# Kernel tuning notes

Hardware: AMD Instinct MI355X
Metric: run time of the kernel (lower is better)

Reference implementation:

```python
import jax, jax.numpy as jnp
import numpy as np

EMB = 1024
HEADS = 16
WINDOW = 128


def setup_inputs() -> dict:
    key = jax.random.key(0)
    ks = jax.random.split(key, 9)
    B, N = 2, 2048
    s = 0.02
    f32 = jnp.float32
    return {
        "x": jax.random.normal(ks[0], (B, N, EMB), dtype=f32),
        "Wq": jax.random.normal(ks[1], (EMB, EMB), dtype=f32) * s,
        "bq": jnp.zeros((EMB,), dtype=f32),
        "Wk": jax.random.normal(ks[2], (EMB, EMB), dtype=f32) * s,
        "bk": jnp.zeros((EMB,), dtype=f32),
        "Wv": jax.random.normal(ks[3], (EMB, EMB), dtype=f32) * s,
        "bv": jnp.zeros((EMB,), dtype=f32),
        "Wp": jax.random.normal(ks[4], (EMB, EMB), dtype=f32) * s,
        "bp": jnp.zeros((EMB,), dtype=f32),
    }


def reference(x, Wq, bq, Wk, bk, Wv, bv, Wp, bp):
    B, N, E = x.shape
    H = HEADS
    d = E // H

    def proj(W, b):
        # torch nn.Linear: y = x @ W^T + b, then split heads -> [b, h, n, d]
        y = jnp.einsum('bne,fe->bnf', x, W) + b
        return y.reshape(B, N, H, d).transpose(0, 2, 1, 3)

    q = proj(Wq, bq)
    k = proj(Wk, bk)
    v = proj(Wv, bv)

    # full QK^T then mask out-of-window entries (faithful to original)
    energy = jnp.einsum('bhqd,bhkd->bhqk', q, k)  # [B,H,N,N]
    idx = jnp.arange(N)
    out_of_window = jnp.abs(idx[:, None] - idx[None, :]) > WINDOW  # [N,N] bool
    fmin = jnp.finfo(jnp.float32).min
    energy = jnp.where(out_of_window, fmin, energy)

    scaling = jnp.sqrt(jnp.float32(E))  # note: original scales by sqrt(emb_size)
    att = jax.nn.softmax(energy / scaling, axis=-1)

    out = jnp.einsum('bhqk,bhkd->bhqd', att, v)  # [B,H,N,d]
    out = out.transpose(0, 2, 1, 3).reshape(B, N, E)
    return jnp.einsum('bne,fe->bnf', out, Wp) + bp
```

## Files before the change

### kernel.cpp

```cpp
#include <hip/hip_runtime.h>
#include <stdint.h>

#define EMB    1024
#define NHEAD  16
#define HDIM   64
#define NSEQ   2048
#define NBATCH 2
#define WINDOW 128
#define MROWS  (NBATCH * NSEQ)

typedef __attribute__((ext_vector_type(8))) short  bf16x8;
typedef __attribute__((ext_vector_type(4))) float  f32x4;
typedef __attribute__((ext_vector_type(4))) short  short4v;

__device__ __forceinline__ unsigned short f2bf(float f) {
  union { float f; uint32_t u; } c; c.f = f;
  uint32_t u = c.u;
  u += 0x7fffu + ((u >> 16) & 1u);
  return (unsigned short)(u >> 16);
}

#define GLOAD16(g, l) __builtin_amdgcn_global_load_lds( \
    (const __attribute__((address_space(1))) void*)(g), \
    (__attribute__((address_space(3))) void*)(l), 16, 0, 0)

__global__ __launch_bounds__(256) void cvt_all(
    const float* __restrict__ x,
    const float* __restrict__ w0, const float* __restrict__ w1,
    const float* __restrict__ w2, const float* __restrict__ w3,
    unsigned short* __restrict__ xb,
    unsigned short* __restrict__ o0, unsigned short* __restrict__ o1,
    unsigned short* __restrict__ o2, unsigned short* __restrict__ o3) {
  const int i = blockIdx.x * 256 + threadIdx.x;
  const float* src; unsigned short* dst; int off;
  if (i < 1048576) { src = x; dst = xb; off = i; }
  else {
    int j = i - 1048576;
    int sel = j >> 18; off = j & 262143;
    src = sel == 0 ? w0 : sel == 1 ? w1 : sel == 2 ? w2 : w3;
    dst = sel == 0 ? o0 : sel == 1 ? o1 : sel == 2 ? o2 : o3;
  }
  float4 v = ((const float4*)src)[off];
  short4v o;
  o.x = (short)f2bf(v.x);
  o.y = (short)f2bf(v.y);
  o.z = (short)f2bf(v.z);
  o.w = (short)f2bf(v.w);
  ((short4v*)dst)[off] = o;
}

__device__ __forceinline__ void gemm_pipe(const unsigned short* __restrict__ A,
                                          const unsigned short* __restrict__ Bw,
                                          const float* __restrict__ bias,
                                          void* __restrict__ Cv,
                                          int m0, int n0, int mode, float scale) {
  constexpr int K = 1024, BK = 64, NT = K / BK;
  __shared__ char lds[2][32768];
  const int t    = threadIdx.x;
  const int lane = t & 63;
  const int wv   = t >> 6;
  const int lhi  = lane >> 4, llo = lane & 15;
  const int wr   = wv >> 1, wc = wv & 1;

  const unsigned short* gsrc[8];
  int ldsoff[8];
  #pragma unroll
  for (int li = 0; li < 8; ++li) {
    const int isB = li >= 4;
    const int c = (isB ? (li - 4) : li) * 4 + wv;
    const int P = c * 1024 + lane * 16;
    const int L = P ^ (((P >> 7) & 7) << 4);
    const int row = L >> 7, sl = (L >> 4) & 7;
    gsrc[li] = (isB ? Bw + (size_t)(n0 + row) * K : A + (size_t)(m0 + row) * K) + sl * 8;
    ldsoff[li] = isB * 16384 + c * 1024;
  }

  int aoff[2][4], boff[2][4];
  #pragma unroll
  for (int ks = 0; ks < 2; ++ks)
    #pragma unroll
    for (int f = 0; f < 4; ++f) {
      const int ar = wr * 64 + f * 16 + llo;
      aoff[ks][f] = (ar * 128 + ks * 64 + lhi * 16) ^ ((ar & 7) << 4);
      const int bc = wc * 64 + f * 16 + llo;
      boff[ks][f] = 16384 + ((bc * 128 + ks * 64 + lhi * 16) ^ ((bc & 7) << 4));
    }

  const f32x4 zero = {0.f, 0.f, 0.f, 0.f};
  f32x4 acc[4][4];
  #pragma unroll
  for (int i = 0; i < 4; ++i)
    #pragma unroll
    for (int j = 0; j < 4; ++j) acc[i][j] = zero;

  #pragma unroll
  for (int li = 0; li < 8; ++li) GLOAD16(gsrc[li], (char*)lds + ldsoff[li]);
  #pragma unroll
  for (int li = 0; li < 8; ++li) GLOAD16(gsrc[li] + BK, (char*)lds + 32768 + ldsoff[li]);

  for (int t0 = 0; t0 < NT; ++t0) {
    if (t0 + 1 < NT) asm volatile("s_waitcnt vmcnt(8)" ::: "memory");
    else             asm volatile("s_waitcnt vmcnt(0)" ::: "memory");
    asm volatile("s_barrier" ::: "memory");
    __builtin_amdgcn_sched_barrier(0);

    const char* base = (const char*)lds + (t0 & 1) * 32768;
    bf16x8 af[2][4], bg[2][4];
    #pragma unroll
    for (int ks = 0; ks < 2; ++ks)
      #pragma unroll
      for (int f = 0; f < 4; ++f) {
        af[ks][f] = *(const bf16x8*)(base + aoff[ks][f]);
        bg[ks][f] = *(const bf16x8*)(base + boff[ks][f]);
      }
    asm volatile("s_waitcnt lgkmcnt(0)" ::: "memory");
    asm volatile("s_barrier" ::: "memory");
    __builtin_amdgcn_sched_barrier(0);

    if (t0 + 2 < NT) {
      #pragma unroll
      for (int li = 0; li < 8; ++li)
        GLOAD16(gsrc[li] + (t0 + 2) * BK, (char*)lds + (t0 & 1) * 32768 + ldsoff[li]);
    }

    __builtin_amdgcn_s_setprio(1);
    #pragma unroll
    for (int ks = 0; ks < 2; ++ks)
      #pragma unroll
      for (int mf = 0; mf < 4; ++mf)
        #pragma unroll
        for (int nf = 0; nf < 4; ++nf)
          acc[mf][nf] = __builtin_amdgcn_mfma_f32_16x16x32_bf16(af[ks][mf], bg[ks][nf], acc[mf][nf], 0, 0, 0);
    __builtin_amdgcn_s_setprio(0);
  }

  const int wm = wr * 64, wn = wc * 64;
  #pragma unroll
  for (int mf = 0; mf < 4; ++mf) {
    #pragma unroll
    for (int nf = 0; nf < 4; ++nf) {
      const int col = n0 + wn + nf * 16 + llo;
      if (mode == 1) {
        const int row_base = m0 + wm + mf * 16 + lhi * 4;
        const int bb = row_base >> 11, n = row_base & 2047;
        const int hh = col >> 6, dd = col & 63;
        short4v o;
        #pragma unroll
        for (int r = 0; r < 4; ++r) o[r] = (short)f2bf((acc[mf][nf][r] + bias[col]) * scale);
        unsigned short* p = (unsigned short*)Cv +
            ((size_t)((bb * NHEAD + hh) * HDIM + dd)) * NSEQ + n;
        *(short4v*)p = o;
      } else {
        #pragma unroll
        for (int r = 0; r < 4; ++r) {
          const int row = m0 + wm + mf * 16 + lhi * 4 + r;
          const float v = (acc[mf][nf][r] + bias[col]) * scale;
          if (mode == 0) {
            const int bb = row >> 11, n = row & 2047;
            const int hh = col >> 6, dd = col & 63;
            ((unsigned short*)Cv)[((size_t)(bb * NHEAD + hh) * NSEQ + n) * HDIM + dd] = f2bf(v);
          } else {
            ((float*)Cv)[(size_t)row * EMB + col] = v;
          }
        }
      }
    }
  }
}

__global__ __launch_bounds__(256, 2) void gemm_qkv(
    const unsigned short* __restrict__ A,
    const unsigned short* __restrict__ W0, const unsigned short* __restrict__ W1,
    const unsigned short* __restrict__ W2,
    const float* __restrict__ b0, const float* __restrict__ b1, const float* __restrict__ b2,
    unsigned short* __restrict__ O0, unsigned short* __restrict__ O1,
    unsigned short* __restrict__ O2) {
  const int m0 = blockIdx.x * 128, n0 = blockIdx.y * 128;
  const unsigned short* W = (blockIdx.z == 0) ? W0 : (blockIdx.z == 1) ? W1 : W2;
  const float* bb         = (blockIdx.z == 0) ? b0 : (blockIdx.z == 1) ? b1 : b2;
  unsigned short* O       = (blockIdx.z == 0) ? O0 : (blockIdx.z == 1) ? O1 : O2;
  const int mode          = (blockIdx.z == 2) ? 1 : 0;
  const float scale       = (blockIdx.z == 0) ? 0.03125f : 1.0f;
  gemm_pipe(A, W, bb, (void*)O, m0, n0, mode, scale);
}

__global__ __launch_bounds__(256, 2) void gemm_proj(
    const unsigned short* __restrict__ A, const unsigned short* __restrict__ W,
    const float* __restrict__ bias, float* __restrict__ O) {
  gemm_pipe(A, W, bias, (void*)O, blockIdx.x * 128, blockIdx.y * 128, 2, 1.0f);
}

__global__ __launch_bounds__(256) void attn_kernel(
    const unsigned short* __restrict__ Qh, const unsigned short* __restrict__ Kh,
    const unsigned short* __restrict__ Vt, unsigned short* __restrict__ AO) {
  __shared__ unsigned short P[4][16 * 32];
  const int t = threadIdx.x;
  const int lane = t & 63, wv = t >> 6;
  const int lhi = lane >> 4, llo = lane & 15;

  const int linear = blockIdx.x + 32 * (blockIdx.y + 16 * blockIdx.z);
  const int xcd = linear & 7, pos = linear >> 3;
  const int plane = xcd * 4 + (pos >> 5);
  const int qblk = pos & 31;
  const int b = plane >> 4, h = plane & 15;
  const int q0 = qblk * 64 + wv * 16;

  const size_t pbase = (size_t)plane * NSEQ * HDIM;

  bf16x8 aq0, aq1;
  {
    const unsigned short* qp = Qh + pbase + (size_t)(q0 + llo) * HDIM + 8 * lhi;
    aq0 = *(const bf16x8*)qp;
    aq1 = *(const bf16x8*)(qp + 32);
  }

  bf16x8 vones;
  #pragma unroll
  for (int j = 0; j < 8; ++j) vones[j] = (short)0x3F80;

  const f32x4 zero = {0.f, 0.f, 0.f, 0.f};
  f32x4 accv[4];
  f32x4 s_acc = zero;
  #pragma unroll
  for (int i = 0; i < 4; ++i) accv[i] = zero;

  #pragma unroll 3
  for (int ct = 0; ct < 9; ++ct) {
    const int kb = q0 - WINDOW + ct * 32;
    f32x4 e[2];
    #pragma unroll
    for (int half = 0; half < 2; ++half) {
      int krow = kb + half * 16 + llo;
      int krc = krow < 0 ? 0 : (krow > NSEQ - 1 ? NSEQ - 1 : krow);
      const unsigned short* kp = Kh + pbase + (size_t)krc * HDIM + 8 * lhi;
      bf16x8 bk0 = *(const bf16x8*)kp;
      bf16x8 bk1 = *(const bf16x8*)(kp + 32);
      f32x4 z = zero;
      z = __builtin_amdgcn_mfma_f32_16x16x32_bf16(aq0, bk0, z, 0, 0, 0);
      z = __builtin_amdgcn_mfma_f32_16x16x32_bf16(aq1, bk1, z, 0, 0, 0);
      e[half] = z;
    }
    f32x4 p0, p1;
    #pragma unroll
    for (int half = 0; half < 2; ++half) {
      const int key = kb + half * 16 + llo;
      #pragma unroll
      for (int r = 0; r < 4; ++r) {
        const int q = q0 + lhi * 4 + r;
        const int dlt = key - q;
        const bool valid = (key >= 0) && (key < NSEQ) && (dlt <= WINDOW) && (dlt >= -WINDOW);
        const float ev = valid ? fminf(e[half][r], 40.f) : -1e30f;
        if (half == 0) p0[r] = __expf(ev); else p1[r] = __expf(ev);
      }
    }

    #pragma unroll
    for (int r = 0; r < 4; ++r) {
      P[wv][(lhi * 4 + r) * 32 + llo]      = f2bf(p0[r]);
      P[wv][(lhi * 4 + r) * 32 + 16 + llo] = f2bf(p1[r]);
    }
    const bf16x8 pa = *(const bf16x8*)&P[wv][llo * 32 + 8 * lhi];

    s_acc = __builtin_amdgcn_mfma_f32_16x16x32_bf16(pa, vones, s_acc, 0, 0, 0);

    {
      int c = kb + 8 * lhi;
      c = c < 0 ? 0 : (c > NSEQ - 8 ? NSEQ - 8 : c);
      #pragma unroll
      for (int fd = 0; fd < 4; ++fd) {
        const unsigned short* vp = Vt + pbase + (size_t)(fd * 16 + llo) * NSEQ + c;
        bf16x8 bv = *(const bf16x8*)vp;
        accv[fd] = __builtin_amdgcn_mfma_f32_16x16x32_bf16(pa, bv, accv[fd], 0, 0, 0);
      }
    }
  }

  #pragma unroll
  for (int fd = 0; fd < 4; ++fd) {
    #pragma unroll
    for (int r = 0; r < 4; ++r) {
      const float o = accv[fd][r] / s_acc[r];
      const int q = q0 + lhi * 4 + r;
      AO[((size_t)b * NSEQ + q) * EMB + h * HDIM + fd * 16 + llo] = f2bf(o);
    }
  }
}

extern "C" void kernel_launch(void* const* d_in, const int* in_sizes, int n_in,
                              void* d_out, int out_size, void* d_ws, size_t ws_size,
                              hipStream_t stream) {
  (void)in_sizes; (void)n_in; (void)out_size; (void)ws_size;
  const float* x  = (const float*)d_in[0];
  const float* Wq = (const float*)d_in[1];
  const float* bq = (const float*)d_in[2];
  const float* Wk = (const float*)d_in[3];
  const float* bk = (const float*)d_in[4];
  const float* Wv = (const float*)d_in[5];
  const float* bv = (const float*)d_in[6];
  const float* Wp = (const float*)d_in[7];
  const float* bp = (const float*)d_in[8];
  float* out = (float*)d_out;
  char* ws = (char*)d_ws;
  const size_t MB = 1u << 20;
  unsigned short* xb  = (unsigned short*)(ws + 0 * MB);
  unsigned short* Wqb = (unsigned short*)(ws + 8 * MB);
  unsigned short* Wkb = (unsigned short*)(ws + 10 * MB);
  unsigned short* Wvb = (unsigned short*)(ws + 12 * MB);
  unsigned short* Wpb = (unsigned short*)(ws + 14 * MB);
  unsigned short* Qb  = (unsigned short*)(ws + 16 * MB);
  unsigned short* Kb  = (unsigned short*)(ws + 24 * MB);
  unsigned short* Vtb = (unsigned short*)(ws + 32 * MB);
  unsigned short* AOb = (unsigned short*)(ws + 40 * MB);

  cvt_all<<<dim3(8192), dim3(256), 0, stream>>>(x, Wq, Wk, Wv, Wp,
                                                xb, Wqb, Wkb, Wvb, Wpb);

  gemm_qkv<<<dim3(MROWS / 128, EMB / 128, 3), dim3(256), 0, stream>>>(
      xb, Wqb, Wkb, Wvb, bq, bk, bv, Qb, Kb, Vtb);

  attn_kernel<<<dim3(NSEQ / 64, NHEAD, NBATCH), dim3(256), 0, stream>>>(Qb, Kb, Vtb, AOb);

  gemm_proj<<<dim3(MROWS / 128, EMB / 128), dim3(256), 0, stream>>>(AOb, Wpb, bp, out);
}
```

Baseline: 97.21 us.

## Use 256x256 tiles with 512 threads and XCD-aware tile remap for QKV GEMM

Replaces the shared 128x128 GEMM path for the QKV projection with a dedicated kernel. It uses 256x256 output tiles, 8 waves per block, and double-buffered 64KB LDS stages. Block indices are remapped so that neighbouring tiles land on the same XCD, for better L2 reuse. The larger tiles raise arithmetic intensity per loaded byte, but they cut the grid to 192 blocks, fewer than the CU count. The 128KB of LDS per block also limits occupancy to one block per CU. The output projection keeps a simplified 128-tile path.

```diff
diff --git a/kernel.cpp b/kernel.cpp
--- a/kernel.cpp
+++ b/kernel.cpp
@@ -49,11 +49,146 @@
   ((short4v*)dst)[off] = o;
 }
 
-__device__ __forceinline__ void gemm_pipe(const unsigned short* __restrict__ A,
-                                          const unsigned short* __restrict__ Bw,
-                                          const float* __restrict__ bias,
-                                          void* __restrict__ Cv,
-                                          int m0, int n0, int mode, float scale) {
+__global__ __launch_bounds__(512, 2) void gemm_qkv(
+    const unsigned short* __restrict__ A,
+    const unsigned short* __restrict__ W0, const unsigned short* __restrict__ W1,
+    const unsigned short* __restrict__ W2,
+    const float* __restrict__ b0, const float* __restrict__ b1, const float* __restrict__ b2,
+    unsigned short* __restrict__ O0, unsigned short* __restrict__ O1,
+    unsigned short* __restrict__ O2) {
+  constexpr int K = 1024, BK = 64, NT = K / BK;
+  __shared__ char lds[2][65536];
+  const int t    = threadIdx.x;
+  const int lane = t & 63;
+  const int wv   = t >> 6;
+  const int lhi  = lane >> 4, llo = lane & 15;
+  const int wr   = wv >> 2, wc = wv & 3;
+
+  const int orig = blockIdx.x + 16 * blockIdx.y + 64 * blockIdx.z;
+  const int tl   = (orig & 7) * 24 + (orig >> 3);
+  const int bx   = tl / 12, rem = tl % 12, by = rem / 3, bz = rem % 3;
+  const int m0   = bx * 256, n0 = by * 256;
+  const unsigned short* Bw = bz == 0 ? W0 : bz == 1 ? W1 : W2;
+  const float* bias        = bz == 0 ? b0 : bz == 1 ? b1 : b2;
+  unsigned short* Cv       = bz == 0 ? (unsigned short*)O0
+                           : bz == 1 ? (unsigned short*)O1 : (unsigned short*)O2;
+  const int   mode  = (bz == 2) ? 1 : 0;
+  const float scale = (bz == 0) ? 0.03125f : 1.0f;
+
+  const unsigned short* gsrc[8];
+  int ldsoff[8];
+  #pragma unroll
+  for (int li = 0; li < 8; ++li) {
+    const int isB = li >= 4;
+    const int P = (li & 3) * 8192 + t * 16;
+    const int L = P ^ (((P >> 7) & 7) << 4);
+    const int row = L >> 7, sl = (L >> 4) & 7;
+    gsrc[li] = (isB ? Bw + (size_t)(n0 + row) * K : A + (size_t)(m0 + row) * K) + sl * 8;
+    ldsoff[li] = isB * 32768 + (li & 3) * 8192 + wv * 1024;
+  }
+
+  int aoff[8], boff[4];
+  #pragma unroll
+  for (int mf = 0; mf < 8; ++mf) {
+    const int ar = wr * 128 + mf * 16 + llo;
+    aoff[mf] = (ar * 128 + lhi * 16) ^ ((ar & 7) << 4);
+  }
+  #pragma unroll
+  for (int nf = 0; nf < 4; ++nf) {
+    const int bc = wc * 64 + nf * 16 + llo;
+    boff[nf] = 32768 + ((bc * 128 + lhi * 16) ^ ((bc & 7) << 4));
+  }
+
+  const f32x4 zero = {0.f, 0.f, 0.f, 0.f};
+  f32x4 acc[8][4];
+  #pragma unroll
+  for (int i = 0; i < 8; ++i)
+    #pragma unroll
+    for (int j = 0; j < 4; ++j) acc[i][j] = zero;
+
+  #pragma unroll
+  for (int li = 0; li < 8; ++li) GLOAD16(gsrc[li], (char*)lds + ldsoff[li]);
+  #pragma unroll
+  for (int li = 0; li < 8; ++li) GLOAD16(gsrc[li] + BK, (char*)lds + 65536 + ldsoff[li]);
+
+  for (int t0 = 0; t0 < NT; ++t0) {
+    if (t0 + 1 < NT) asm volatile("s_waitcnt vmcnt(8)" ::: "memory");
+    else             asm volatile("s_waitcnt vmcnt(0)" ::: "memory");
+    asm volatile("s_barrier" ::: "memory");
+    __builtin_amdgcn_sched_barrier(0);
+
+    const char* base = (const char*)lds + (t0 & 1) * 65536;
+
+    bf16x8 a0[8], bg0[4];
+    #pragma unroll
+    for (int mf = 0; mf < 8; ++mf) a0[mf] = *(const bf16x8*)(base + aoff[mf]);
+    #pragma unroll
+    for (int nf = 0; nf < 4; ++nf) bg0[nf] = *(const bf16x8*)(base + boff[nf]);
+    __builtin_amdgcn_s_setprio(1);
+    #pragma unroll
+    for (int mf = 0; mf < 8; ++mf)
+      #pragma unroll
+      for (int nf = 0; nf < 4; ++nf)
+        acc[mf][nf] = __builtin_amdgcn_mfma_f32_16x16x32_bf16(a0[mf], bg0[nf], acc[mf][nf], 0, 0, 0);
+    __builtin_amdgcn_s_setprio(0);
+
+    bf16x8 a1[8], bg1[4];
+    #pragma unroll
+    for (int mf = 0; mf < 8; ++mf) a1[mf] = *(const bf16x8*)(base + (aoff[mf] ^ 64));
+    #pragma unroll
+    for (int nf = 0; nf < 4; ++nf) bg1[nf] = *(const bf16x8*)(base + (boff[nf] ^ 64));
+    asm volatile("s_waitcnt lgkmcnt(0)" ::: "memory");
+    asm volatile("s_barrier" ::: "memory");
+    __builtin_amdgcn_sched_barrier(0);
+
+    if (t0 + 2 < NT) {
+      #pragma unroll
+      for (int li = 0; li < 8; ++li)
+        GLOAD16(gsrc[li] + (t0 + 2) * BK, (char*)lds + (t0 & 1) * 65536 + ldsoff[li]);
+    }
+
+    __builtin_amdgcn_s_setprio(1);
+    #pragma unroll
+    for (int mf = 0; mf < 8; ++mf)
+      #pragma unroll
+      for (int nf = 0; nf < 4; ++nf)
+        acc[mf][nf] = __builtin_amdgcn_mfma_f32_16x16x32_bf16(a1[mf], bg1[nf], acc[mf][nf], 0, 0, 0);
+    __builtin_amdgcn_s_setprio(0);
+  }
+
+  #pragma unroll
+  for (int mf = 0; mf < 8; ++mf) {
+    #pragma unroll
+    for (int nf = 0; nf < 4; ++nf) {
+      const int col = n0 + wc * 64 + nf * 16 + llo;
+      if (mode == 1) {
+        const int row_base = m0 + wr * 128 + mf * 16 + lhi * 4;
+        const int bb = row_base >> 11, n = row_base & 2047;
+        const int hh = col >> 6, dd = col & 63;
+        short4v o;
+        #pragma unroll
+        for (int r = 0; r < 4; ++r) o[r] = (short)f2bf(acc[mf][nf][r] + bias[col]);
+        unsigned short* p = Cv + ((size_t)((bb * NHEAD + hh) * HDIM + dd)) * NSEQ + n;
+        *(short4v*)p = o;
+      } else {
+        #pragma unroll
+        for (int r = 0; r < 4; ++r) {
+          const int row = m0 + wr * 128 + mf * 16 + lhi * 4 + r;
+          const float v = (acc[mf][nf][r] + bias[col]) * scale;
+          const int bb = row >> 11, n = row & 2047;
+          const int hh = col >> 6, dd = col & 63;
+          Cv[((size_t)(bb * NHEAD + hh) * NSEQ + n) * HDIM + dd] = f2bf(v);
+        }
+      }
+    }
+  }
+}
+
+__device__ __forceinline__ void gemm_pipe128(const unsigned short* __restrict__ A,
+                                             const unsigned short* __restrict__ Bw,
+                                             const float* __restrict__ bias,
+                                             float* __restrict__ Cv,
+                                             int m0, int n0) {
   constexpr int K = 1024, BK = 64, NT = K / BK;
   __shared__ char lds[2][32768];
   const int t    = threadIdx.x;
@@ -140,54 +275,19 @@
     #pragma unroll
     for (int nf = 0; nf < 4; ++nf) {
       const int col = n0 + wn + nf * 16 + llo;
-      if (mode == 1) {
-        const int row_base = m0 + wm + mf * 16 + lhi * 4;
-        const int bb = row_base >> 11, n = row_base & 2047;
-        const int hh = col >> 6, dd = col & 63;
-        short4v o;
-        #pragma unroll
-        for (int r = 0; r < 4; ++r) o[r] = (short)f2bf((acc[mf][nf][r] + bias[col]) * scale);
-        unsigned short* p = (unsigned short*)Cv +
-            ((size_t)((bb * NHEAD + hh) * HDIM + dd)) * NSEQ + n;
-        *(short4v*)p = o;
-      } else {
-        #pragma unroll
-        for (int r = 0; r < 4; ++r) {
-          const int row = m0 + wm + mf * 16 + lhi * 4 + r;
-          const float v = (acc[mf][nf][r] + bias[col]) * scale;
-          if (mode == 0) {
-            const int bb = row >> 11, n = row & 2047;
-            const int hh = col >> 6, dd = col & 63;
-            ((unsigned short*)Cv)[((size_t)(bb * NHEAD + hh) * NSEQ + n) * HDIM + dd] = f2bf(v);
-          } else {
-            ((float*)Cv)[(size_t)row * EMB + col] = v;
-          }
-        }
+      #pragma unroll
+      for (int r = 0; r < 4; ++r) {
+        const int row = m0 + wm + mf * 16 + lhi * 4 + r;
+        Cv[(size_t)row * EMB + col] = acc[mf][nf][r] + bias[col];
       }
     }
   }
-}
-
-__global__ __launch_bounds__(256, 2) void gemm_qkv(
-    const unsigned short* __restrict__ A,
-    const unsigned short* __restrict__ W0, const unsigned short* __restrict__ W1,
-    const unsigned short* __restrict__ W2,
-    const float* __restrict__ b0, const float* __restrict__ b1, const float* __restrict__ b2,
-    unsigned short* __restrict__ O0, unsigned short* __restrict__ O1,
-    unsigned short* __restrict__ O2) {
-  const int m0 = blockIdx.x * 128, n0 = blockIdx.y * 128;
-  const unsigned short* W = (blockIdx.z == 0) ? W0 : (blockIdx.z == 1) ? W1 : W2;
-  const float* bb         = (blockIdx.z == 0) ? b0 : (blockIdx.z == 1) ? b1 : b2;
-  unsigned short* O       = (blockIdx.z == 0) ? O0 : (blockIdx.z == 1) ? O1 : O2;
-  const int mode          = (blockIdx.z == 2) ? 1 : 0;
-  const float scale       = (blockIdx.z == 0) ? 0.03125f : 1.0f;
-  gemm_pipe(A, W, bb, (void*)O, m0, n0, mode, scale);
 }
 
 __global__ __launch_bounds__(256, 2) void gemm_proj(
     const unsigned short* __restrict__ A, const unsigned short* __restrict__ W,
     const float* __restrict__ bias, float* __restrict__ O) {
-  gemm_pipe(A, W, bias, (void*)O, blockIdx.x * 128, blockIdx.y * 128, 2, 1.0f);
+  gemm_pipe128(A, W, bias, O, blockIdx.x * 128, blockIdx.y * 128);
 }
 
 __global__ __launch_bounds__(256) void attn_kernel(
@@ -315,7 +415,7 @@
   cvt_all<<<dim3(8192), dim3(256), 0, stream>>>(x, Wq, Wk, Wv, Wp,
                                                 xb, Wqb, Wkb, Wvb, Wpb);
 
-  gemm_qkv<<<dim3(MROWS / 128, EMB / 128, 3), dim3(256), 0, stream>>>(
+  gemm_qkv<<<dim3(MROWS / 256, EMB / 256, 3), dim3(512), 0, stream>>>(
       xb, Wqb, Wkb, Wvb, bq, bk, bv, Qb, Kb, Vtb);
 
   attn_kernel<<<dim3(NSEQ / 64, NHEAD, NBATCH), dim3(256), 0, stream>>>(Qb, Kb, Vtb, AOb);
```

After: 101.1 us. +4.0%, slower.

## Split attention key window across two waves per query tile and combine via LDS

Applied to the files above, without the earlier changes.

Doubles the attention block to 512 threads so each 16-query tile is handled by two waves, each covering part of the 9 key chunks (4 and 5). The second wave writes its partial numerator and denominator to shared memory, and after a barrier the first wave adds them and writes the output. This shortens the serial chain of MFMA and exp work per wave and raises wave-level parallelism, at the cost of extra LDS traffic, a block barrier and imbalanced halves. Because softmax is unnormalized with a fixed clamp, adding the partial sums is exact.

```diff
diff --git a/kernel.cpp b/kernel.cpp
--- a/kernel.cpp
+++ b/kernel.cpp
@@ -190,20 +190,22 @@
   gemm_pipe(A, W, bias, (void*)O, blockIdx.x * 128, blockIdx.y * 128, 2, 1.0f);
 }
 
-__global__ __launch_bounds__(256) void attn_kernel(
+__global__ __launch_bounds__(512, 8) void attn_kernel(
     const unsigned short* __restrict__ Qh, const unsigned short* __restrict__ Kh,
     const unsigned short* __restrict__ Vt, unsigned short* __restrict__ AO) {
-  __shared__ unsigned short P[4][16 * 32];
+  __shared__ unsigned short P[8][16 * 32];
+  __shared__ float comb[4][20][64];
   const int t = threadIdx.x;
   const int lane = t & 63, wv = t >> 6;
   const int lhi = lane >> 4, llo = lane & 15;
+  const int qsub = wv >> 1, half = wv & 1;
 
   const int linear = blockIdx.x + 32 * (blockIdx.y + 16 * blockIdx.z);
   const int xcd = linear & 7, pos = linear >> 3;
   const int plane = xcd * 4 + (pos >> 5);
   const int qblk = pos & 31;
   const int b = plane >> 4, h = plane & 15;
-  const int q0 = qblk * 64 + wv * 16;
+  const int q0 = qblk * 64 + qsub * 16;
 
   const size_t pbase = (size_t)plane * NSEQ * HDIM;
 
@@ -224,13 +226,12 @@
   #pragma unroll
   for (int i = 0; i < 4; ++i) accv[i] = zero;
 
-  #pragma unroll 3
-  for (int ct = 0; ct < 9; ++ct) {
+  auto do_chunk = [&](int ct) {
     const int kb = q0 - WINDOW + ct * 32;
     f32x4 e[2];
     #pragma unroll
-    for (int half = 0; half < 2; ++half) {
-      int krow = kb + half * 16 + llo;
+    for (int hf = 0; hf < 2; ++hf) {
+      int krow = kb + hf * 16 + llo;
       int krc = krow < 0 ? 0 : (krow > NSEQ - 1 ? NSEQ - 1 : krow);
       const unsigned short* kp = Kh + pbase + (size_t)krc * HDIM + 8 * lhi;
       bf16x8 bk0 = *(const bf16x8*)kp;
@@ -238,19 +239,19 @@
       f32x4 z = zero;
       z = __builtin_amdgcn_mfma_f32_16x16x32_bf16(aq0, bk0, z, 0, 0, 0);
       z = __builtin_amdgcn_mfma_f32_16x16x32_bf16(aq1, bk1, z, 0, 0, 0);
-      e[half] = z;
+      e[hf] = z;
     }
     f32x4 p0, p1;
     #pragma unroll
-    for (int half = 0; half < 2; ++half) {
-      const int key = kb + half * 16 + llo;
+    for (int hf = 0; hf < 2; ++hf) {
+      const int key = kb + hf * 16 + llo;
       #pragma unroll
       for (int r = 0; r < 4; ++r) {
         const int q = q0 + lhi * 4 + r;
         const int dlt = key - q;
         const bool valid = (key >= 0) && (key < NSEQ) && (dlt <= WINDOW) && (dlt >= -WINDOW);
-        const float ev = valid ? fminf(e[half][r], 40.f) : -1e30f;
-        if (half == 0) p0[r] = __expf(ev); else p1[r] = __expf(ev);
+        const float ev = valid ? fminf(e[hf][r], 40.f) : -1e30f;
+        if (hf == 0) p0[r] = __expf(ev); else p1[r] = __expf(ev);
       }
     }
 
@@ -263,25 +264,48 @@
 
     s_acc = __builtin_amdgcn_mfma_f32_16x16x32_bf16(pa, vones, s_acc, 0, 0, 0);
 
-    {
-      int c = kb + 8 * lhi;
-      c = c < 0 ? 0 : (c > NSEQ - 8 ? NSEQ - 8 : c);
-      #pragma unroll
-      for (int fd = 0; fd < 4; ++fd) {
-        const unsigned short* vp = Vt + pbase + (size_t)(fd * 16 + llo) * NSEQ + c;
-        bf16x8 bv = *(const bf16x8*)vp;
-        accv[fd] = __builtin_amdgcn_mfma_f32_16x16x32_bf16(pa, bv, accv[fd], 0, 0, 0);
+    int c = kb + 8 * lhi;
+    c = c < 0 ? 0 : (c > NSEQ - 8 ? NSEQ - 8 : c);
+    #pragma unroll
+    for (int fd = 0; fd < 4; ++fd) {
+      const unsigned short* vp = Vt + pbase + (size_t)(fd * 16 + llo) * NSEQ + c;
+      bf16x8 bv = *(const bf16x8*)vp;
+      accv[fd] = __builtin_amdgcn_mfma_f32_16x16x32_bf16(pa, bv, accv[fd], 0, 0, 0);
+    }
+  };
+
+  if (half == 0) {
+    #pragma unroll 2
+    for (int ct = 0; ct < 4; ++ct) do_chunk(ct);
+  } else {
+    #pragma unroll 2
+    for (int ct = 4; ct < 9; ++ct) do_chunk(ct);
+    #pragma unroll
+    for (int i = 0; i < 4; ++i)
+      #pragma unroll
+      for (int r = 0; r < 4; ++r)
+        comb[qsub][i * 4 + r][lane] = accv[i][r];
+    #pragma unroll
+    for (int r = 0; r < 4; ++r) comb[qsub][16 + r][lane] = s_acc[r];
+  }
+  __syncthreads();
+  if (half == 0) {
+    #pragma unroll
+    for (int i = 0; i < 4; ++i)
+      #pragma unroll
+      for (int r = 0; r < 4; ++r)
+        accv[i][r] += comb[qsub][i * 4 + r][lane];
+    #pragma unroll
+    for (int r = 0; r < 4; ++r) s_acc[r] += comb[qsub][16 + r][lane];
+
+    #pragma unroll
+    for (int fd = 0; fd < 4; ++fd) {
+      #pragma unroll
+      for (int r = 0; r < 4; ++r) {
+        const float o = accv[fd][r] / s_acc[r];
+        const int q = q0 + lhi * 4 + r;
+        AO[((size_t)b * NSEQ + q) * EMB + h * HDIM + fd * 16 + llo] = f2bf(o);
       }
-    }
-  }
-
-  #pragma unroll
-  for (int fd = 0; fd < 4; ++fd) {
-    #pragma unroll
-    for (int r = 0; r < 4; ++r) {
-      const float o = accv[fd][r] / s_acc[r];
-      const int q = q0 + lhi * 4 + r;
-      AO[((size_t)b * NSEQ + q) * EMB + h * HDIM + fd * 16 + llo] = f2bf(o);
     }
   }
 }
@@ -318,7 +342,7 @@
   gemm_qkv<<<dim3(MROWS / 128, EMB / 128, 3), dim3(256), 0, stream>>>(
       xb, Wqb, Wkb, Wvb, bq, bk, bv, Qb, Kb, Vtb);
 
-  attn_kernel<<<dim3(NSEQ / 64, NHEAD, NBATCH), dim3(256), 0, stream>>>(Qb, Kb, Vtb, AOb);
+  attn_kernel<<<dim3(NSEQ / 64, NHEAD, NBATCH), dim3(512), 0, stream>>>(Qb, Kb, Vtb, AOb);
 
   gemm_proj<<<dim3(MROWS / 128, EMB / 128), dim3(256), 0, stream>>>(AOb, Wpb, bp, out);
 }
```

New measurement: 111.3 us. +14.5%, slower.

## Stage shared K/V tiles in LDS with double-buffered async loads in attention

Applied to the files above, without the earlier changes.

The attention kernel now loads each 32-key K tile and matching V^T tile once per block into swizzled LDS with global_load_lds, double-buffered across iterations. The four waves share those tiles instead of each issuing its own global loads. The loop now spans 10 chunks over the block's 64-query range plus the window, where it used to cover 9 per wave, so each wave does some extra masked work. It also adds barriers per iteration and sets a launch-bounds occupancy hint of 4.

```diff
diff --git a/kernel.cpp b/kernel.cpp
--- a/kernel.cpp
+++ b/kernel.cpp
@@ -190,10 +190,12 @@
   gemm_pipe(A, W, bias, (void*)O, blockIdx.x * 128, blockIdx.y * 128, 2, 1.0f);
 }
 
-__global__ __launch_bounds__(256) void attn_kernel(
+__global__ __launch_bounds__(256, 4) void attn_kernel(
     const unsigned short* __restrict__ Qh, const unsigned short* __restrict__ Kh,
     const unsigned short* __restrict__ Vt, unsigned short* __restrict__ AO) {
-  __shared__ unsigned short P[4][16 * 32];
+  constexpr int NCH = 10;
+  __shared__ char kv[2][8192];
+  __shared__ unsigned short Pb[4][16 * 32];
   const int t = threadIdx.x;
   const int lane = t & 63, wv = t >> 6;
   const int lhi = lane >> 4, llo = lane & 15;
@@ -203,7 +205,8 @@
   const int plane = xcd * 4 + (pos >> 5);
   const int qblk = pos & 31;
   const int b = plane >> 4, h = plane & 15;
-  const int q0 = qblk * 64 + wv * 16;
+  const int q0b = qblk * 64;
+  const int q0 = q0b + wv * 16;
 
   const size_t pbase = (size_t)plane * NSEQ * HDIM;
 
@@ -214,6 +217,27 @@
     aq1 = *(const bf16x8*)(qp + 32);
   }
 
+  const int PK = t * 16;
+  const int LK = PK ^ (((PK >> 7) & 7) << 4);
+  const int krow_l = LK >> 7;
+  const int kslot8 = ((LK >> 4) & 7) * 8;
+  const int LV = PK ^ (((PK >> 7) & 3) << 4);
+  const int vrow = LV >> 6;
+  const int vslot8 = ((LV >> 4) & 3) * 8;
+
+  int koff[2];
+  #pragma unroll
+  for (int half = 0; half < 2; ++half) {
+    const int row = half * 16 + llo;
+    koff[half] = (row * 128 + lhi * 16) ^ ((row & 7) << 4);
+  }
+  int voff[4];
+  #pragma unroll
+  for (int fd = 0; fd < 4; ++fd) {
+    const int row = fd * 16 + llo;
+    voff[fd] = 4096 + ((row * 64 + lhi * 16) ^ (((row >> 1) & 3) << 4));
+  }
+
   bf16x8 vones;
   #pragma unroll
   for (int j = 0; j < 8; ++j) vones[j] = (short)0x3F80;
@@ -224,20 +248,48 @@
   #pragma unroll
   for (int i = 0; i < 4; ++i) accv[i] = zero;
 
-  #pragma unroll 3
-  for (int ct = 0; ct < 9; ++ct) {
-    const int kb = q0 - WINDOW + ct * 32;
+  auto stage = [&](int ct, int slot) {
+    const int kb = q0b - WINDOW + ct * 32;
+    int n = kb + krow_l;
+    n = n < 0 ? 0 : (n > NSEQ - 1 ? NSEQ - 1 : n);
+    GLOAD16(Kh + pbase + (size_t)n * HDIM + kslot8, (char*)kv[slot] + PK);
+    int c = kb + vslot8;
+    c = c < 0 ? 0 : (c > NSEQ - 8 ? NSEQ - 8 : c);
+    GLOAD16(Vt + pbase + (size_t)vrow * NSEQ + c, (char*)kv[slot] + 4096 + PK);
+  };
+
+  stage(0, 0);
+  stage(1, 1);
+
+  for (int ct = 0; ct < NCH; ++ct) {
+    if (ct + 1 < NCH) asm volatile("s_waitcnt vmcnt(2)" ::: "memory");
+    else              asm volatile("s_waitcnt vmcnt(0)" ::: "memory");
+    asm volatile("s_barrier" ::: "memory");
+    __builtin_amdgcn_sched_barrier(0);
+
+    const char* sb = kv[ct & 1];
+    bf16x8 bk[2][2], bv[4];
+    #pragma unroll
+    for (int half = 0; half < 2; ++half) {
+      bk[half][0] = *(const bf16x8*)(sb + koff[half]);
+      bk[half][1] = *(const bf16x8*)(sb + (koff[half] ^ 64));
+    }
+    #pragma unroll
+    for (int fd = 0; fd < 4; ++fd) bv[fd] = *(const bf16x8*)(sb + voff[fd]);
+    asm volatile("s_waitcnt lgkmcnt(0)" ::: "memory");
+    __builtin_amdgcn_sched_barrier(0);
+    asm volatile("s_barrier" ::: "memory");
+    __builtin_amdgcn_sched_barrier(0);
+
+    if (ct + 2 < NCH) stage(ct + 2, ct & 1);
+
+    const int kb = q0b - WINDOW + ct * 32;
     f32x4 e[2];
     #pragma unroll
     for (int half = 0; half < 2; ++half) {
-      int krow = kb + half * 16 + llo;
-      int krc = krow < 0 ? 0 : (krow > NSEQ - 1 ? NSEQ - 1 : krow);
-      const unsigned short* kp = Kh + pbase + (size_t)krc * HDIM + 8 * lhi;
-      bf16x8 bk0 = *(const bf16x8*)kp;
-      bf16x8 bk1 = *(const bf16x8*)(kp + 32);
       f32x4 z = zero;
-      z = __builtin_amdgcn_mfma_f32_16x16x32_bf16(aq0, bk0, z, 0, 0, 0);
-      z = __builtin_amdgcn_mfma_f32_16x16x32_bf16(aq1, bk1, z, 0, 0, 0);
+      z = __builtin_amdgcn_mfma_f32_16x16x32_bf16(aq0, bk[half][0], z, 0, 0, 0);
+      z = __builtin_amdgcn_mfma_f32_16x16x32_bf16(aq1, bk[half][1], z, 0, 0, 0);
       e[half] = z;
     }
     f32x4 p0, p1;
@@ -256,23 +308,15 @@
 
     #pragma unroll
     for (int r = 0; r < 4; ++r) {
-      P[wv][(lhi * 4 + r) * 32 + llo]      = f2bf(p0[r]);
-      P[wv][(lhi * 4 + r) * 32 + 16 + llo] = f2bf(p1[r]);
-    }
-    const bf16x8 pa = *(const bf16x8*)&P[wv][llo * 32 + 8 * lhi];
+      Pb[wv][(lhi * 4 + r) * 32 + llo]      = f2bf(p0[r]);
+      Pb[wv][(lhi * 4 + r) * 32 + 16 + llo] = f2bf(p1[r]);
+    }
+    const bf16x8 pa = *(const bf16x8*)&Pb[wv][llo * 32 + 8 * lhi];
 
     s_acc = __builtin_amdgcn_mfma_f32_16x16x32_bf16(pa, vones, s_acc, 0, 0, 0);
-
-    {
-      int c = kb + 8 * lhi;
-      c = c < 0 ? 0 : (c > NSEQ - 8 ? NSEQ - 8 : c);
-      #pragma unroll
-      for (int fd = 0; fd < 4; ++fd) {
-        const unsigned short* vp = Vt + pbase + (size_t)(fd * 16 + llo) * NSEQ + c;
-        bf16x8 bv = *(const bf16x8*)vp;
-        accv[fd] = __builtin_amdgcn_mfma_f32_16x16x32_bf16(pa, bv, accv[fd], 0, 0, 0);
-      }
-    }
+    #pragma unroll
+    for (int fd = 0; fd < 4; ++fd)
+      accv[fd] = __builtin_amdgcn_mfma_f32_16x16x32_bf16(pa, bv[fd], accv[fd], 0, 0, 0);
   }
 
   #pragma unroll
```

New measurement: 80.55 us. -17.1%, faster.
